# Kernel tuning notes

Hardware: AMD Instinct MI355X
Metric: run time of the kernel (lower is better)

## Reference

```python
import jax, jax.numpy as jnp
import numpy as np

GROUPS = 4
PPG = 16  # kv_channels // groups = 64 // 4
Q_CH = 256
KV_CH = 64


def setup_inputs() -> dict:
    key = jax.random.key(0)
    ks = jax.random.split(key, 7)
    N, T, L = 4, 64, 64
    q = jax.random.normal(ks[0], (N, L, L, Q_CH), dtype=jnp.float32)
    kv = jax.random.normal(ks[1], (N, T, L, L, KV_CH), dtype=jnp.float32)
    # torch nn.Linear weights, stored pre-transposed so y = x @ W
    s_q = 1.0 / np.sqrt(Q_CH)
    s_kv = 1.0 / np.sqrt(KV_CH)
    Wq = jax.random.uniform(ks[2], (Q_CH, KV_CH), jnp.float32, -s_q, s_q)
    Wk = jax.random.uniform(ks[3], (KV_CH, KV_CH), jnp.float32, -s_kv, s_kv)
    Wv = jax.random.uniform(ks[4], (KV_CH, KV_CH), jnp.float32, -s_kv, s_kv)
    Wout = jax.random.uniform(ks[5], (KV_CH, Q_CH), jnp.float32, -s_kv, s_kv)
    b_out = jax.random.uniform(ks[6], (Q_CH,), jnp.float32, -s_kv, s_kv)
    return {"q": q, "kv": kv, "Wq": Wq, "Wk": Wk, "Wv": Wv, "Wout": Wout, "b_out": b_out}


def reference(q, kv, Wq, Wk, Wv, Wout, b_out):
    N, L, _, _ = q.shape
    T = kv.shape[1]
    qh = (q @ Wq).reshape(N, L, L, GROUPS, PPG)                 # nijgc
    kh = (kv @ Wk).reshape(N, T, L, L, GROUPS, PPG)             # ntijgc
    vh = (kv @ Wv).reshape(N, T, L, L, GROUPS, PPG)             # ntijgc
    scale = 1.0 / jnp.sqrt(jnp.float32(PPG))
    attn = jnp.einsum('nijgc,ntijgc->ntijg', qh, kh) * scale    # scores over T per pixel
    attn = jax.nn.softmax(attn, axis=1)
    x = jnp.einsum('ntijg,ntijgc->nijgc', attn, vh).reshape(N, L, L, KV_CH)
    return x @ Wout + b_out
```

## Files before the change

### kernel.cpp

```cpp
#include <hip/hip_runtime.h>

typedef short short8 __attribute__((ext_vector_type(8)));
typedef float f32x4 __attribute__((ext_vector_type(4)));

__device__ __forceinline__ float bf2f(unsigned short u) {
  union { unsigned int i; float f; } v; v.i = ((unsigned int)u) << 16; return v.f;
}
__device__ __forceinline__ unsigned short f2bf(float f) {
  unsigned int x = __float_as_uint(f);
  unsigned int r = (x + 0x7fffu + ((x >> 16) & 1u)) >> 16;
  return (unsigned short)r;
}

typedef __attribute__((address_space(1))) void* gas_t;
typedef __attribute__((address_space(3))) void* las_t;
__device__ __forceinline__ void async16(const float* g, float* l) {
  __builtin_amdgcn_global_load_lds((gas_t)g, (las_t)l, 16, 0, 0);
}

template <int N>
__device__ __forceinline__ void wait_vm() {
  asm volatile("s_waitcnt vmcnt(%0)" :: "n"(N) : "memory");
  __builtin_amdgcn_sched_barrier(0);
}

__global__ __launch_bounds__(256) void prep_kernel(
    const float* __restrict__ Wq, const float* __restrict__ Wk,
    const float* __restrict__ Wv, const float* __restrict__ Wout,
    unsigned short* __restrict__ Afrag, unsigned short* __restrict__ WVOfrag) {
  const int b = blockIdx.x, tid = threadIdx.x;
  if (b < 256) {
    const int p = b, g = tid >> 6, d = tid & 63;
    float s = 0.f;
#pragma unroll
    for (int c = 0; c < 16; ++c)
      s += Wq[p * 64 + g * 16 + c] * Wk[d * 64 + g * 16 + c];
    s *= 0.25f;
    const int n = g * 64 + d, k = p;
    Afrag[(size_t)(k >> 5) * 8192 + n * 32 + (k & 31)] = f2bf(s);
  } else {
    const int row = b - 256, g = row >> 6, d = row & 63, q = tid;
    float s = 0.f;
#pragma unroll
    for (int c = 0; c < 16; ++c)
      s += Wv[d * 64 + g * 16 + c] * Wout[(g * 16 + c) * 256 + q];
    WVOfrag[(size_t)(row >> 5) * 8192 + q * 32 + (row & 31)] = f2bf(s);
  }
}

__global__ __launch_bounds__(256, 1) void fused_kernel(
    const float* __restrict__ q, const float* __restrict__ kv,
    const unsigned short* __restrict__ Afrag,
    const unsigned short* __restrict__ WVOfrag,
    const float* __restrict__ bias, float* __restrict__ Out) {
  __shared__ float kvbuf[6][4096];
  __shared__ unsigned short qk_s[64 * 256];
  __shared__ unsigned short A_s[64 * 40];

  const int tid = threadIdx.x;
  const int wgid = blockIdx.x;
  const int w = tid >> 6, lane = tid & 63;
  const int m_l = lane & 15, quad = lane >> 4;
  const int j = tid >> 2, g = tid & 3;

  {
    const float* qrow = q + (size_t)wgid * 64 * 256;
    const int srow = tid >> 2, sc = (tid & 3) * 8;
    f32x4 acc[16];
#pragma unroll
    for (int i = 0; i < 16; ++i) acc[i] = (f32x4){0.f, 0.f, 0.f, 0.f};
    for (int ks = 0; ks < 8; ++ks) {
      const float4* xp = (const float4*)(qrow + (size_t)srow * 256 + ks * 32 + sc);
      float4 x0 = xp[0], x1 = xp[1];
      short8 vv;
      vv[0] = (short)f2bf(x0.x); vv[1] = (short)f2bf(x0.y);
      vv[2] = (short)f2bf(x0.z); vv[3] = (short)f2bf(x0.w);
      vv[4] = (short)f2bf(x1.x); vv[5] = (short)f2bf(x1.y);
      vv[6] = (short)f2bf(x1.z); vv[7] = (short)f2bf(x1.w);
      *(short8*)&A_s[srow * 40 + sc] = vv;
      __syncthreads();
      short8 a = *(const short8*)&A_s[(w * 16 + m_l) * 40 + quad * 8];
#pragma unroll
      for (int nt = 0; nt < 16; ++nt) {
        short8 bf = *(const short8*)(Afrag +
            ((size_t)ks * 256 + nt * 16 + m_l) * 32 + quad * 8);
        acc[nt] = __builtin_amdgcn_mfma_f32_16x16x32_bf16(a, bf, acc[nt], 0, 0, 0);
      }
      __syncthreads();
    }
#pragma unroll
    for (int nt = 0; nt < 16; ++nt) {
      const int col = nt * 16 + m_l;
#pragma unroll
      for (int r = 0; r < 4; ++r)
        qk_s[(w * 16 + quad * 4 + r) * 256 + col] = f2bf(acc[nt][r]);
    }
  }

  const float* kvblk =
      kv + ((size_t)(wgid >> 6) << 24) + ((size_t)(wgid & 63) << 12);
  const int loff = w * 1024 + lane * 4;

#pragma unroll
  for (int tt = 0; tt < 5; ++tt) {
    const float* src = kvblk + ((size_t)tt << 18) + loff;
    float* dst = &kvbuf[tt][loff];
#pragma unroll
    for (int qq = 0; qq < 4; ++qq) async16(src + qq * 256, dst + qq * 256);
  }

  float qf[64];
#pragma unroll
  for (int c = 0; c < 16; ++c) {
    const int rot = (c + j) & 15;
    uint2 u = *(const uint2*)&qk_s[j * 256 + g * 64 + rot * 4];
    qf[4 * c + 0] = bf2f((unsigned short)(u.x & 0xffffu));
    qf[4 * c + 1] = bf2f((unsigned short)(u.x >> 16));
    qf[4 * c + 2] = bf2f((unsigned short)(u.y & 0xffffu));
    qf[4 * c + 3] = bf2f((unsigned short)(u.y >> 16));
  }

  float yac[64];
#pragma unroll
  for (int c = 0; c < 64; ++c) yac[c] = 0.f;
  float lsum = 0.f;

  auto stepT = [&](int bb) {
    const float* row = &kvbuf[bb][j * 64];
    float s = 0.f;
    float4 cv[16];
#pragma unroll
    for (int c = 0; c < 16; ++c) {
      const int rot = (c + j) & 15;
      cv[c] = *(const float4*)(row + rot * 4);
      s = fmaf(cv[c].x, qf[4 * c + 0], s);
      s = fmaf(cv[c].y, qf[4 * c + 1], s);
      s = fmaf(cv[c].z, qf[4 * c + 2], s);
      s = fmaf(cv[c].w, qf[4 * c + 3], s);
    }
    const float p = __expf(s);
    lsum += p;
#pragma unroll
    for (int c = 0; c < 16; ++c) {
      yac[4 * c + 0] = fmaf(p, cv[c].x, yac[4 * c + 0]);
      yac[4 * c + 1] = fmaf(p, cv[c].y, yac[4 * c + 1]);
      yac[4 * c + 2] = fmaf(p, cv[c].z, yac[4 * c + 2]);
      yac[4 * c + 3] = fmaf(p, cv[c].w, yac[4 * c + 3]);
    }
  };

  int b = 0, ib = 5;
#pragma unroll 1
  for (int t = 0; t < 59; ++t) {
    wait_vm<16>();
    const float* src = kvblk + ((size_t)(t + 5) << 18) + loff;
    float* dst = &kvbuf[ib][loff];
#pragma unroll
    for (int qq = 0; qq < 4; ++qq) async16(src + qq * 256, dst + qq * 256);
    stepT(b);
    b = (b == 5) ? 0 : b + 1;
    ib = (ib == 5) ? 0 : ib + 1;
  }
  wait_vm<16>(); stepT(5);
  wait_vm<12>(); stepT(0);
  wait_vm<8>();  stepT(1);
  wait_vm<4>();  stepT(2);
  wait_vm<0>();  stepT(3);

  {
    const float inv = 1.f / lsum;
    unsigned int* yst = (unsigned int*)qk_s;
#pragma unroll
    for (int c = 0; c < 16; ++c) {
      const int rot = (c + j) & 15;
      uint2 pk;
      pk.x = (unsigned int)f2bf(yac[4 * c + 0] * inv) |
             ((unsigned int)f2bf(yac[4 * c + 1] * inv) << 16);
      pk.y = (unsigned int)f2bf(yac[4 * c + 2] * inv) |
             ((unsigned int)f2bf(yac[4 * c + 3] * inv) << 16);
      *(uint2*)&yst[j * 128 + g * 32 + rot * 2] = pk;
    }
  }
  __syncthreads();

  {
    f32x4 acc[16];
#pragma unroll
    for (int i = 0; i < 16; ++i) acc[i] = (f32x4){0.f, 0.f, 0.f, 0.f};
    for (int ks = 0; ks < 8; ++ks) {
      short8 a = *(const short8*)&qk_s[(w * 16 + m_l) * 256 + ks * 32 + quad * 8];
#pragma unroll
      for (int nt = 0; nt < 16; ++nt) {
        short8 bf = *(const short8*)(WVOfrag +
            ((size_t)ks * 256 + nt * 16 + m_l) * 32 + quad * 8);
        acc[nt] = __builtin_amdgcn_mfma_f32_16x16x32_bf16(a, bf, acc[nt], 0, 0, 0);
      }
    }
    float* outb = Out + (size_t)wgid * 64 * 256;
#pragma unroll
    for (int nt = 0; nt < 16; ++nt) {
      const int col = nt * 16 + m_l;
      const float bb = bias[col];
#pragma unroll
      for (int r = 0; r < 4; ++r)
        outb[(size_t)(w * 16 + quad * 4 + r) * 256 + col] = acc[nt][r] + bb;
    }
  }
}

extern "C" void kernel_launch(void* const* d_in, const int* in_sizes, int n_in,
                              void* d_out, int out_size, void* d_ws,
                              size_t ws_size, hipStream_t stream) {
  const float* q    = (const float*)d_in[0];
  const float* kv   = (const float*)d_in[1];
  const float* Wq   = (const float*)d_in[2];
  const float* Wk   = (const float*)d_in[3];
  const float* Wv   = (const float*)d_in[4];
  const float* Wout = (const float*)d_in[5];
  const float* bout = (const float*)d_in[6];

  unsigned short* ws      = (unsigned short*)d_ws;
  unsigned short* Afrag   = ws;
  unsigned short* WVOfrag = ws + 65536;

  hipLaunchKernelGGL(prep_kernel, dim3(512), dim3(256), 0, stream,
                     Wq, Wk, Wv, Wout, Afrag, WVOfrag);
  hipLaunchKernelGGL(fused_kernel, dim3(256), dim3(256), 0, stream,
                     q, kv, Afrag, WVOfrag, bout, (float*)d_out);
}
```

Before: 406.0 us.

## Split each row across two workgroups, halving per-thread state for higher occupancy

Each workgroup now handles 32 pixels instead of 64, and the grid doubles to 512 workgroups. Each pixel-group's 64-channel dot product is split across two threads that combine partial scores with a lane shuffle, which halves register and LDS usage and allows two workgroups per CU. The q projection GEMM is restructured so each wave computes 4 column tiles over 32 rows in one pass with a padded LDS layout, and the kv prefetch is issued before that GEMM so loading overlaps it. The ring buffer shrinks to 5 slots of half size. The costs are an extra shuffle per timestep and redundant exp work in paired lanes.

```diff
diff --git a/kernel.cpp b/kernel.cpp
--- a/kernel.cpp
+++ b/kernel.cpp
@@ -48,100 +48,115 @@
   }
 }
 
-__global__ __launch_bounds__(256, 1) void fused_kernel(
+__global__ __launch_bounds__(256, 2) void fused_kernel(
     const float* __restrict__ q, const float* __restrict__ kv,
     const unsigned short* __restrict__ Afrag,
     const unsigned short* __restrict__ WVOfrag,
     const float* __restrict__ bias, float* __restrict__ Out) {
-  __shared__ float kvbuf[6][4096];
-  __shared__ unsigned short qk_s[64 * 256];
-  __shared__ unsigned short A_s[64 * 40];
+  __shared__ float kvbuf[5][2048];
+  __shared__ unsigned short qk_s[32 * 264];
+  __shared__ unsigned short qA_s[32 * 264];
 
   const int tid = threadIdx.x;
   const int wgid = blockIdx.x;
   const int w = tid >> 6, lane = tid & 63;
   const int m_l = lane & 15, quad = lane >> 4;
-  const int j = tid >> 2, g = tid & 3;
-
-  {
-    const float* qrow = q + (size_t)wgid * 64 * 256;
-    const int srow = tid >> 2, sc = (tid & 3) * 8;
-    f32x4 acc[16];
-#pragma unroll
-    for (int i = 0; i < 16; ++i) acc[i] = (f32x4){0.f, 0.f, 0.f, 0.f};
-    for (int ks = 0; ks < 8; ++ks) {
-      const float4* xp = (const float4*)(qrow + (size_t)srow * 256 + ks * 32 + sc);
-      float4 x0 = xp[0], x1 = xp[1];
+
+  const float* kvbase = kv + ((size_t)(wgid >> 7) << 24) +
+                        ((size_t)((wgid >> 1) & 63) << 12) +
+                        ((size_t)(wgid & 1) << 11);
+  const int loff = w * 512 + lane * 4;
+
+#pragma unroll
+  for (int tt = 0; tt < 4; ++tt) {
+    const float* src = kvbase + ((size_t)tt << 18) + loff;
+    float* dst = &kvbuf[tt][loff];
+    async16(src, dst);
+    async16(src + 256, dst + 256);
+  }
+
+  {
+    const float* qrow = q + (size_t)(wgid >> 1) * 16384 + (size_t)(wgid & 1) * 8192;
+    const int r = tid >> 3, cc = (tid & 7) * 32;
+    const float4* xp = (const float4*)(qrow + r * 256 + cc);
+#pragma unroll
+    for (int kk = 0; kk < 4; ++kk) {
+      float4 x0 = xp[2 * kk], x1 = xp[2 * kk + 1];
       short8 vv;
       vv[0] = (short)f2bf(x0.x); vv[1] = (short)f2bf(x0.y);
       vv[2] = (short)f2bf(x0.z); vv[3] = (short)f2bf(x0.w);
       vv[4] = (short)f2bf(x1.x); vv[5] = (short)f2bf(x1.y);
       vv[6] = (short)f2bf(x1.z); vv[7] = (short)f2bf(x1.w);
-      *(short8*)&A_s[srow * 40 + sc] = vv;
-      __syncthreads();
-      short8 a = *(const short8*)&A_s[(w * 16 + m_l) * 40 + quad * 8];
-#pragma unroll
-      for (int nt = 0; nt < 16; ++nt) {
+      *(short8*)&qA_s[r * 264 + cc + kk * 8] = vv;
+    }
+  }
+  __syncthreads();
+  {
+    f32x4 acc[2][4];
+#pragma unroll
+    for (int mt = 0; mt < 2; ++mt)
+#pragma unroll
+      for (int ntl = 0; ntl < 4; ++ntl) acc[mt][ntl] = (f32x4){0.f, 0.f, 0.f, 0.f};
+#pragma unroll
+    for (int ks = 0; ks < 8; ++ks) {
+      short8 a0 = *(const short8*)&qA_s[m_l * 264 + ks * 32 + quad * 8];
+      short8 a1 = *(const short8*)&qA_s[(16 + m_l) * 264 + ks * 32 + quad * 8];
+#pragma unroll
+      for (int ntl = 0; ntl < 4; ++ntl) {
         short8 bf = *(const short8*)(Afrag +
-            ((size_t)ks * 256 + nt * 16 + m_l) * 32 + quad * 8);
-        acc[nt] = __builtin_amdgcn_mfma_f32_16x16x32_bf16(a, bf, acc[nt], 0, 0, 0);
-      }
-      __syncthreads();
-    }
-#pragma unroll
-    for (int nt = 0; nt < 16; ++nt) {
-      const int col = nt * 16 + m_l;
-#pragma unroll
-      for (int r = 0; r < 4; ++r)
-        qk_s[(w * 16 + quad * 4 + r) * 256 + col] = f2bf(acc[nt][r]);
-    }
-  }
-
-  const float* kvblk =
-      kv + ((size_t)(wgid >> 6) << 24) + ((size_t)(wgid & 63) << 12);
-  const int loff = w * 1024 + lane * 4;
-
-#pragma unroll
-  for (int tt = 0; tt < 5; ++tt) {
-    const float* src = kvblk + ((size_t)tt << 18) + loff;
-    float* dst = &kvbuf[tt][loff];
-#pragma unroll
-    for (int qq = 0; qq < 4; ++qq) async16(src + qq * 256, dst + qq * 256);
-  }
-
-  float qf[64];
-#pragma unroll
-  for (int c = 0; c < 16; ++c) {
-    const int rot = (c + j) & 15;
-    uint2 u = *(const uint2*)&qk_s[j * 256 + g * 64 + rot * 4];
+            ((size_t)ks * 256 + (w * 4 + ntl) * 16 + m_l) * 32 + quad * 8);
+        acc[0][ntl] = __builtin_amdgcn_mfma_f32_16x16x32_bf16(a0, bf, acc[0][ntl], 0, 0, 0);
+        acc[1][ntl] = __builtin_amdgcn_mfma_f32_16x16x32_bf16(a1, bf, acc[1][ntl], 0, 0, 0);
+      }
+    }
+#pragma unroll
+    for (int mt = 0; mt < 2; ++mt)
+#pragma unroll
+      for (int ntl = 0; ntl < 4; ++ntl) {
+        const int col = (w * 4 + ntl) * 16 + m_l;
+#pragma unroll
+        for (int r4 = 0; r4 < 4; ++r4)
+          qk_s[(mt * 16 + quad * 4 + r4) * 264 + col] = f2bf(acc[mt][ntl][r4]);
+      }
+  }
+  __syncthreads();
+
+  const int jl = tid >> 3, sub = tid & 7, g = sub >> 1, h = sub & 1;
+
+  float qf[32];
+#pragma unroll
+  for (int c = 0; c < 8; ++c) {
+    const int rot = (c + jl) & 7;
+    uint2 u = *(const uint2*)&qk_s[jl * 264 + g * 64 + h * 32 + rot * 4];
     qf[4 * c + 0] = bf2f((unsigned short)(u.x & 0xffffu));
     qf[4 * c + 1] = bf2f((unsigned short)(u.x >> 16));
     qf[4 * c + 2] = bf2f((unsigned short)(u.y & 0xffffu));
     qf[4 * c + 3] = bf2f((unsigned short)(u.y >> 16));
   }
 
-  float yac[64];
-#pragma unroll
-  for (int c = 0; c < 64; ++c) yac[c] = 0.f;
+  float yac[32];
+#pragma unroll
+  for (int c = 0; c < 32; ++c) yac[c] = 0.f;
   float lsum = 0.f;
 
-  auto stepT = [&](int bb) {
-    const float* row = &kvbuf[bb][j * 64];
+  auto stepT = [&](int slot) {
+    const float* row = &kvbuf[slot][jl * 64 + h * 32];
     float s = 0.f;
-    float4 cv[16];
-#pragma unroll
-    for (int c = 0; c < 16; ++c) {
-      const int rot = (c + j) & 15;
+    float4 cv[8];
+#pragma unroll
+    for (int c = 0; c < 8; ++c) {
+      const int rot = (c + jl) & 7;
       cv[c] = *(const float4*)(row + rot * 4);
       s = fmaf(cv[c].x, qf[4 * c + 0], s);
       s = fmaf(cv[c].y, qf[4 * c + 1], s);
       s = fmaf(cv[c].z, qf[4 * c + 2], s);
       s = fmaf(cv[c].w, qf[4 * c + 3], s);
     }
-    const float p = __expf(s);
+    const float so = __shfl_xor(s, 1, 64);
+    const float p = __expf(s + so);
     lsum += p;
 #pragma unroll
-    for (int c = 0; c < 16; ++c) {
+    for (int c = 0; c < 8; ++c) {
       yac[4 * c + 0] = fmaf(p, cv[c].x, yac[4 * c + 0]);
       yac[4 * c + 1] = fmaf(p, cv[c].y, yac[4 * c + 1]);
       yac[4 * c + 2] = fmaf(p, cv[c].z, yac[4 * c + 2]);
@@ -149,62 +164,67 @@
     }
   };
 
-  int b = 0, ib = 5;
+  int sb = 0, si = 4;
 #pragma unroll 1
-  for (int t = 0; t < 59; ++t) {
-    wait_vm<16>();
-    const float* src = kvblk + ((size_t)(t + 5) << 18) + loff;
-    float* dst = &kvbuf[ib][loff];
-#pragma unroll
-    for (int qq = 0; qq < 4; ++qq) async16(src + qq * 256, dst + qq * 256);
-    stepT(b);
-    b = (b == 5) ? 0 : b + 1;
-    ib = (ib == 5) ? 0 : ib + 1;
-  }
-  wait_vm<16>(); stepT(5);
-  wait_vm<12>(); stepT(0);
-  wait_vm<8>();  stepT(1);
-  wait_vm<4>();  stepT(2);
-  wait_vm<0>();  stepT(3);
+  for (int t = 0; t < 60; ++t) {
+    wait_vm<6>();
+    const float* src = kvbase + ((size_t)(t + 4) << 18) + loff;
+    float* dst = &kvbuf[si][loff];
+    async16(src, dst);
+    async16(src + 256, dst + 256);
+    stepT(sb);
+    sb = (sb == 4) ? 0 : sb + 1;
+    si = (si == 4) ? 0 : si + 1;
+  }
+  wait_vm<6>(); stepT(0);
+  wait_vm<4>(); stepT(1);
+  wait_vm<2>(); stepT(2);
+  wait_vm<0>(); stepT(3);
 
   {
     const float inv = 1.f / lsum;
-    unsigned int* yst = (unsigned int*)qk_s;
-#pragma unroll
-    for (int c = 0; c < 16; ++c) {
-      const int rot = (c + j) & 15;
+#pragma unroll
+    for (int c = 0; c < 8; ++c) {
+      const int rot = (c + jl) & 7;
       uint2 pk;
       pk.x = (unsigned int)f2bf(yac[4 * c + 0] * inv) |
              ((unsigned int)f2bf(yac[4 * c + 1] * inv) << 16);
       pk.y = (unsigned int)f2bf(yac[4 * c + 2] * inv) |
              ((unsigned int)f2bf(yac[4 * c + 3] * inv) << 16);
-      *(uint2*)&yst[j * 128 + g * 32 + rot * 2] = pk;
+      *(uint2*)&qk_s[jl * 264 + g * 64 + h * 32 + rot * 4] = pk;
     }
   }
   __syncthreads();
 
   {
-    f32x4 acc[16];
-#pragma unroll
-    for (int i = 0; i < 16; ++i) acc[i] = (f32x4){0.f, 0.f, 0.f, 0.f};
+    f32x4 acc[2][4];
+#pragma unroll
+    for (int mt = 0; mt < 2; ++mt)
+#pragma unroll
+      for (int ntl = 0; ntl < 4; ++ntl) acc[mt][ntl] = (f32x4){0.f, 0.f, 0.f, 0.f};
+#pragma unroll
     for (int ks = 0; ks < 8; ++ks) {
-      short8 a = *(const short8*)&qk_s[(w * 16 + m_l) * 256 + ks * 32 + quad * 8];
-#pragma unroll
-      for (int nt = 0; nt < 16; ++nt) {
+      short8 a0 = *(const short8*)&qk_s[m_l * 264 + ks * 32 + quad * 8];
+      short8 a1 = *(const short8*)&qk_s[(16 + m_l) * 264 + ks * 32 + quad * 8];
+#pragma unroll
+      for (int ntl = 0; ntl < 4; ++ntl) {
         short8 bf = *(const short8*)(WVOfrag +
-            ((size_t)ks * 256 + nt * 16 + m_l) * 32 + quad * 8);
-        acc[nt] = __builtin_amdgcn_mfma_f32_16x16x32_bf16(a, bf, acc[nt], 0, 0, 0);
-      }
-    }
-    float* outb = Out + (size_t)wgid * 64 * 256;
-#pragma unroll
-    for (int nt = 0; nt < 16; ++nt) {
-      const int col = nt * 16 + m_l;
-      const float bb = bias[col];
-#pragma unroll
-      for (int r = 0; r < 4; ++r)
-        outb[(size_t)(w * 16 + quad * 4 + r) * 256 + col] = acc[nt][r] + bb;
-    }
+            ((size_t)ks * 256 + (w * 4 + ntl) * 16 + m_l) * 32 + quad * 8);
+        acc[0][ntl] = __builtin_amdgcn_mfma_f32_16x16x32_bf16(a0, bf, acc[0][ntl], 0, 0, 0);
+        acc[1][ntl] = __builtin_amdgcn_mfma_f32_16x16x32_bf16(a1, bf, acc[1][ntl], 0, 0, 0);
+      }
+    }
+    float* outb = Out + (size_t)(wgid >> 1) * 16384 + (size_t)(wgid & 1) * 8192;
+#pragma unroll
+    for (int mt = 0; mt < 2; ++mt)
+#pragma unroll
+      for (int ntl = 0; ntl < 4; ++ntl) {
+        const int col = (w * 4 + ntl) * 16 + m_l;
+        const float bb = bias[col];
+#pragma unroll
+        for (int r4 = 0; r4 < 4; ++r4)
+          outb[(size_t)(mt * 16 + quad * 4 + r4) * 256 + col] = acc[mt][ntl][r4] + bb;
+      }
   }
 }
 
@@ -225,6 +245,6 @@
 
   hipLaunchKernelGGL(prep_kernel, dim3(512), dim3(256), 0, stream,
                      Wq, Wk, Wv, Wout, Afrag, WVOfrag);
-  hipLaunchKernelGGL(fused_kernel, dim3(256), dim3(256), 0, stream,
+  hipLaunchKernelGGL(fused_kernel, dim3(512), dim3(256), 0, stream,
                      q, kv, Afrag, WVOfrag, bout, (float*)d_out);
 }
```

Result: faster. 387.3 us, median of 2 (-4.6%).
